# Performance work log

Measured on AMD Instinct MI355X. Metric: run time of the kernel, lower is better.

The kernel has to match this reference:

```python
import jax, jax.numpy as jnp
import numpy as np

OCC_SIZE = (200, 200, 16)  # n_query = 640000
N_CAM, C, H, W = 6, 128, 64, 176


def setup_inputs() -> dict:
    key = jax.random.key(0)
    k1, k2, k3 = jax.random.split(key, 3)
    n_query = OCC_SIZE[0] * OCC_SIZE[1] * OCC_SIZE[2]
    img_feats = jax.random.normal(k1, (N_CAM, C, H, W), dtype=jnp.float32)
    # pixel coords: x in [0, W-1], y in [0, H-1] (in-range, as the torch code assumes)
    uv = jax.random.uniform(k2, (N_CAM, n_query, 2), dtype=jnp.float32)
    points = uv * jnp.array([W - 1, H - 1], dtype=jnp.float32)
    valid = jax.random.bernoulli(k3, 0.3, (N_CAM, n_query))
    return {"img_feats": img_feats, "points": points, "valid": valid}


def reference(img_feats, points, valid):
    # Faithful to fast_voxel_fill: sequential per-camera masked writes mean the
    n_cam, n_channels = img_feats.shape[0], img_feats.shape[1]
    n_query = points.shape[-2]
    x = jnp.round(points[..., 0]).astype(jnp.int32)  # [n_cam, n_query] -> W index
    y = jnp.round(points[..., 1]).astype(jnp.int32)  # [n_cam, n_query] -> H index
    cam_ids = jnp.arange(n_cam, dtype=jnp.int32)[:, None]
    sel = jnp.max(jnp.where(valid, cam_ids, -1), axis=0)  # [n_query], -1 = no valid cam
    any_valid = sel >= 0
    cam = jnp.maximum(sel, 0)
    q = jnp.arange(n_query)
    xs = x[cam, q]
    ys = y[cam, q]
    gathered = img_feats[cam, :, ys, xs]  # [n_query, C]
    volume = jnp.where(any_valid[:, None], gathered, 0.0).T  # [C, n_query]
    return volume.reshape(n_channels, OCC_SIZE[0], OCC_SIZE[1], OCC_SIZE[2])
```

## Files before the change

kernel.cpp:

```cpp
#include <hip/hip_runtime.h>

#define NCAM 6
#define CCH  128
#define IH   64
#define IW   176
#define NQ   640000
#define PIX  (IH * IW)
#define QT   32
#define LSTRIDE 129

typedef float f32x2 __attribute__((ext_vector_type(2)));
typedef float f32x4 __attribute__((ext_vector_type(4)));

__global__ __launch_bounds__(256) void transpose_kernel(
    const float* __restrict__ in, float* __restrict__ out) {
    __shared__ float tile[32][33];
    const int cam   = blockIdx.z;
    const int pbase = blockIdx.x * 32;
    const int cbase = blockIdx.y * 32;
    const int tx = threadIdx.x, ty = threadIdx.y;

    const float* src = in  + (size_t)cam * CCH * PIX;
    float*       dst = out + (size_t)cam * PIX * CCH;

    #pragma unroll
    for (int j = 0; j < 4; ++j) {
        int c = cbase + ty + j * 8;
        tile[ty + j * 8][tx] =
            __builtin_nontemporal_load(&src[(size_t)c * PIX + (pbase + tx)]);
    }
    __syncthreads();
    #pragma unroll
    for (int j = 0; j < 4; ++j) {
        int p = pbase + ty + j * 8;
        dst[(size_t)p * CCH + (cbase + tx)] = tile[tx][ty + j * 8];
    }
}

__global__ __launch_bounds__(256, 8) void gather_lds_kernel(
    const float* __restrict__ imgT,
    const float* __restrict__ points,
    const int*   __restrict__ valid,
    float*       __restrict__ out) {
    __shared__ float feat[QT * LSTRIDE];
    __shared__ int   sbase[QT];
    __shared__ float sscale[QT];

    const int t     = threadIdx.x;
    const int qbase = blockIdx.x * QT;

    if (t < QT) {
        const int q = qbase + t;
        int sel = -1;
        #pragma unroll
        for (int cam = 0; cam < NCAM; ++cam)
            if (__builtin_nontemporal_load(&valid[(size_t)cam * NQ + q]) != 0)
                sel = cam;
        const int cam = (sel >= 0) ? sel : 0;
        sscale[t] = (sel >= 0) ? 1.0f : 0.0f;
        const f32x2 pt = __builtin_nontemporal_load(
            (const f32x2*)points + (size_t)cam * NQ + q);
        const int x = __float2int_rn(pt.x);
        const int y = __float2int_rn(pt.y);
        sbase[t] = ((cam * IH + y) * IW + x) * CCH;
    }
    __syncthreads();

    {
        const int grp  = t >> 5;
        const int lane = t & 31;
        #pragma unroll
        for (int i = 0; i < 4; ++i) {
            const int ql = i * 8 + grp;
            const float s = sscale[ql];
            const f32x4 v = *((const f32x4*)(imgT + sbase[ql]) + lane);
            const int w = ql * LSTRIDE + 4 * lane;
            feat[w + 0] = v.x * s;
            feat[w + 1] = v.y * s;
            feat[w + 2] = v.z * s;
            feat[w + 3] = v.w * s;
        }
    }
    __syncthreads();

    {
        const int l    = t & 63;
        const int wv   = t >> 6;
        const int qq   = l & 7;
        const int csub = l >> 3;
        #pragma unroll
        for (int iter = 0; iter < 4; ++iter) {
            const int c    = iter * 32 + wv * 8 + csub;
            const int qoff = 4 * qq;
            f32x4 v;
            v.x = feat[(qoff + 0) * LSTRIDE + c];
            v.y = feat[(qoff + 1) * LSTRIDE + c];
            v.z = feat[(qoff + 2) * LSTRIDE + c];
            v.w = feat[(qoff + 3) * LSTRIDE + c];
            __builtin_nontemporal_store(
                v, (f32x4*)(out + (size_t)c * NQ + qbase + qoff));
        }
    }
}

__global__ __launch_bounds__(256) void gather_direct_kernel(
    const float* __restrict__ img,
    const float* __restrict__ points,
    const int*   __restrict__ valid,
    float*       __restrict__ out) {
    const int q = blockIdx.x * 256 + threadIdx.x;

    int sel = -1;
    #pragma unroll
    for (int cam = 0; cam < NCAM; ++cam)
        if (valid[(size_t)cam * NQ + q] != 0) sel = cam;

    const float scale = (sel >= 0) ? 1.0f : 0.0f;
    const int cam = (sel >= 0) ? sel : 0;

    const float2 pt = ((const float2*)points)[(size_t)cam * NQ + q];
    const int x = __float2int_rn(pt.x);
    const int y = __float2int_rn(pt.y);

    const float* src = img + ((size_t)cam * CCH * IH + y) * IW + x;
    #pragma unroll 8
    for (int c = 0; c < CCH; ++c)
        out[(size_t)c * NQ + q] = src[(size_t)c * PIX] * scale;
}

extern "C" void kernel_launch(void* const* d_in, const int* in_sizes, int n_in,
                              void* d_out, int out_size, void* d_ws, size_t ws_size,
                              hipStream_t stream) {
    const float* img    = (const float*)d_in[0];
    const float* points = (const float*)d_in[1];
    const int*   valid  = (const int*)  d_in[2];
    float*       out    = (float*)d_out;

    const size_t need = (size_t)NCAM * CCH * IH * IW * sizeof(float);
    if (ws_size >= need) {
        float* imgT = (float*)d_ws;
        dim3 tb(32, 8, 1);
        dim3 tg(PIX / 32, CCH / 32, NCAM);
        transpose_kernel<<<tg, tb, 0, stream>>>(img, imgT);
        gather_lds_kernel<<<NQ / QT, 256, 0, stream>>>(imgT, points, valid, out);
    } else {
        gather_direct_kernel<<<NQ / 256, 256, 0, stream>>>(img, points, valid, out);
    }
}
```

Baseline: 416.2 us.

## Double-buffer gather tiles so gather loads overlap transposed output stores

Turns the one-tile-per-block gather into a persistent loop in which each block handles 8 query tiles. Two LDS buffers let the next tile's index resolution and global gathers be issued before the current tile's transposed output is stored. The aim is to hide gather latency behind store traffic and cut block launch overhead. The cost is a doubled LDS footprint, occupancy lowered to 4 blocks, and a grid eight times smaller. Any race on the shared buffers is avoided only by the single barrier in each iteration.

New measurement: 436.6 us. 4.9% more time.

```diff
diff --git a/kernel.cpp b/kernel.cpp
--- a/kernel.cpp
+++ b/kernel.cpp
@@ -7,6 +7,8 @@
 #define NQ   640000
 #define PIX  (IH * IW)
 #define QT   32
+#define NT   8
+#define NBLK (NQ / (QT * NT))
 #define LSTRIDE 129
 
 typedef float f32x2 __attribute__((ext_vector_type(2)));
@@ -37,69 +39,92 @@
     }
 }
 
-__global__ __launch_bounds__(256, 8) void gather_lds_kernel(
+__global__ __launch_bounds__(256, 4) void gather_pipe_kernel(
     const float* __restrict__ imgT,
     const float* __restrict__ points,
     const int*   __restrict__ valid,
     float*       __restrict__ out) {
-    __shared__ float feat[QT * LSTRIDE];
-    __shared__ int   sbase[QT];
-    __shared__ float sscale[QT];
+    __shared__ float feat[2][QT * LSTRIDE];
+    __shared__ int   sbase[2][QT];
+    __shared__ float sscale[2][QT];
 
     const int t     = threadIdx.x;
-    const int qbase = blockIdx.x * QT;
+    const int grp   = t >> 5;
+    const int lane  = t & 31;
+    const int tile0 = blockIdx.x * NT;
 
-    if (t < QT) {
-        const int q = qbase + t;
+    auto resolve = [&](int tile, int slot) {
+        const int q = tile * QT + t;
         int sel = -1;
         #pragma unroll
         for (int cam = 0; cam < NCAM; ++cam)
             if (__builtin_nontemporal_load(&valid[(size_t)cam * NQ + q]) != 0)
                 sel = cam;
         const int cam = (sel >= 0) ? sel : 0;
-        sscale[t] = (sel >= 0) ? 1.0f : 0.0f;
+        sscale[slot][t] = (sel >= 0) ? 1.0f : 0.0f;
         const f32x2 pt = __builtin_nontemporal_load(
             (const f32x2*)points + (size_t)cam * NQ + q);
         const int x = __float2int_rn(pt.x);
         const int y = __float2int_rn(pt.y);
-        sbase[t] = ((cam * IH + y) * IW + x) * CCH;
-    }
-    __syncthreads();
+        sbase[slot][t] = ((cam * IH + y) * IW + x) * CCH;
+    };
 
-    {
-        const int grp  = t >> 5;
-        const int lane = t & 31;
+    f32x4 r[4];
+
+    auto issue = [&](int slot) {
         #pragma unroll
         for (int i = 0; i < 4; ++i) {
             const int ql = i * 8 + grp;
-            const float s = sscale[ql];
-            const f32x4 v = *((const f32x4*)(imgT + sbase[ql]) + lane);
+            r[i] = *((const f32x4*)(imgT + sbase[slot][ql]) + lane);
+        }
+    };
+    auto commit = [&](int slot) {
+        #pragma unroll
+        for (int i = 0; i < 4; ++i) {
+            const int ql = i * 8 + grp;
+            const float s = sscale[slot][ql];
             const int w = ql * LSTRIDE + 4 * lane;
-            feat[w + 0] = v.x * s;
-            feat[w + 1] = v.y * s;
-            feat[w + 2] = v.z * s;
-            feat[w + 3] = v.w * s;
+            feat[slot][w + 0] = r[i].x * s;
+            feat[slot][w + 1] = r[i].y * s;
+            feat[slot][w + 2] = r[i].z * s;
+            feat[slot][w + 3] = r[i].w * s;
         }
-    }
+    };
+
+    if (t < QT) resolve(tile0, 0);
     __syncthreads();
+    issue(0);
+    commit(0);
 
-    {
-        const int l    = t & 63;
-        const int wv   = t >> 6;
-        const int qq   = l & 7;
-        const int csub = l >> 3;
-        #pragma unroll
-        for (int iter = 0; iter < 4; ++iter) {
-            const int c    = iter * 32 + wv * 8 + csub;
-            const int qoff = 4 * qq;
-            f32x4 v;
-            v.x = feat[(qoff + 0) * LSTRIDE + c];
-            v.y = feat[(qoff + 1) * LSTRIDE + c];
-            v.z = feat[(qoff + 2) * LSTRIDE + c];
-            v.w = feat[(qoff + 3) * LSTRIDE + c];
-            __builtin_nontemporal_store(
-                v, (f32x4*)(out + (size_t)c * NQ + qbase + qoff));
+    int cur = 0;
+    for (int tt = 0; tt < NT; ++tt) {
+        const int nxt = cur ^ 1;
+        if (tt + 1 < NT && t < QT) resolve(tile0 + tt + 1, nxt);
+        __syncthreads();
+        if (tt + 1 < NT) issue(nxt);
+
+        {
+            const int qbase = (tile0 + tt) * QT;
+            const int l    = t & 63;
+            const int wv   = t >> 6;
+            const int qq   = l & 7;
+            const int csub = l >> 3;
+            #pragma unroll
+            for (int iter = 0; iter < 4; ++iter) {
+                const int c    = iter * 32 + wv * 8 + csub;
+                const int qoff = 4 * qq;
+                f32x4 v;
+                v.x = feat[cur][(qoff + 0) * LSTRIDE + c];
+                v.y = feat[cur][(qoff + 1) * LSTRIDE + c];
+                v.z = feat[cur][(qoff + 2) * LSTRIDE + c];
+                v.w = feat[cur][(qoff + 3) * LSTRIDE + c];
+                __builtin_nontemporal_store(
+                    v, (f32x4*)(out + (size_t)c * NQ + qbase + qoff));
+            }
         }
+
+        if (tt + 1 < NT) commit(nxt);
+        cur = nxt;
     }
 }
 
@@ -142,7 +167,7 @@
         dim3 tb(32, 8, 1);
         dim3 tg(PIX / 32, CCH / 32, NCAM);
         transpose_kernel<<<tg, tb, 0, stream>>>(img, imgT);
-        gather_lds_kernel<<<NQ / QT, 256, 0, stream>>>(imgT, points, valid, out);
+        gather_pipe_kernel<<<NBLK, 256, 0, stream>>>(imgT, points, valid, out);
     } else {
         gather_direct_kernel<<<NQ / 256, 256, 0, stream>>>(img, points, valid, out);
     }
```

## Widen gather tile to 128 queries and stage channels in two halves

Applied to the files above, without the earlier changes.

The gather kernel now handles 128 queries per 512-thread block instead of 32 per 256. It stages the 128 channels in two 64-channel halves through a smaller padded LDS tile. Each output row write becomes a 256-byte contiguous segment per channel instead of 128 bytes, which should improve store coalescing for the output-bound transpose-scatter. The cost is an extra pair of barriers per half, plus the per-query setup still being done by only 128 threads.

Measured after the change: 407.9 us. 2.0% less time.

```diff
diff --git a/kernel.cpp b/kernel.cpp
--- a/kernel.cpp
+++ b/kernel.cpp
@@ -6,8 +6,9 @@
 #define IW   176
 #define NQ   640000
 #define PIX  (IH * IW)
-#define QT   32
-#define LSTRIDE 129
+#define QT   128
+#define CHALF 64
+#define FSTR  67
 
 typedef float f32x2 __attribute__((ext_vector_type(2)));
 typedef float f32x4 __attribute__((ext_vector_type(4)));
@@ -37,12 +38,12 @@
     }
 }
 
-__global__ __launch_bounds__(256, 8) void gather_lds_kernel(
+__global__ __launch_bounds__(512, 8) void gather_wide_kernel(
     const float* __restrict__ imgT,
     const float* __restrict__ points,
     const int*   __restrict__ valid,
     float*       __restrict__ out) {
-    __shared__ float feat[QT * LSTRIDE];
+    __shared__ float feat[QT * FSTR];
     __shared__ int   sbase[QT];
     __shared__ float sscale[QT];
 
@@ -66,40 +67,46 @@
     }
     __syncthreads();
 
-    {
-        const int grp  = t >> 5;
-        const int lane = t & 31;
+    const int grp16  = t >> 4;
+    const int lane16 = t & 15;
+    const int l      = t & 63;
+    const int wv     = t >> 6;
+    const int qq     = l & 15;
+    const int csub   = l >> 4;
+
+    #pragma unroll
+    for (int h = 0; h < 2; ++h) {
         #pragma unroll
         for (int i = 0; i < 4; ++i) {
-            const int ql = i * 8 + grp;
+            const int ql = i * 32 + grp16;
             const float s = sscale[ql];
-            const f32x4 v = *((const f32x4*)(imgT + sbase[ql]) + lane);
-            const int w = ql * LSTRIDE + 4 * lane;
+            const f32x4 v =
+                *((const f32x4*)(imgT + sbase[ql] + h * CHALF) + lane16);
+            const int w = ql * FSTR + 4 * lane16;
             feat[w + 0] = v.x * s;
             feat[w + 1] = v.y * s;
             feat[w + 2] = v.z * s;
             feat[w + 3] = v.w * s;
         }
-    }
-    __syncthreads();
+        __syncthreads();
 
-    {
-        const int l    = t & 63;
-        const int wv   = t >> 6;
-        const int qq   = l & 7;
-        const int csub = l >> 3;
         #pragma unroll
-        for (int iter = 0; iter < 4; ++iter) {
-            const int c    = iter * 32 + wv * 8 + csub;
-            const int qoff = 4 * qq;
-            f32x4 v;
-            v.x = feat[(qoff + 0) * LSTRIDE + c];
-            v.y = feat[(qoff + 1) * LSTRIDE + c];
-            v.z = feat[(qoff + 2) * LSTRIDE + c];
-            v.w = feat[(qoff + 3) * LSTRIDE + c];
-            __builtin_nontemporal_store(
-                v, (f32x4*)(out + (size_t)c * NQ + qbase + qoff));
+        for (int qh = 0; qh < 2; ++qh) {
+            #pragma unroll
+            for (int iter = 0; iter < 2; ++iter) {
+                const int cl   = iter * 32 + wv * 4 + csub;
+                const int c    = h * CHALF + cl;
+                const int qoff = qh * 64 + 4 * qq;
+                f32x4 v;
+                v.x = feat[(qoff + 0) * FSTR + cl];
+                v.y = feat[(qoff + 1) * FSTR + cl];
+                v.z = feat[(qoff + 2) * FSTR + cl];
+                v.w = feat[(qoff + 3) * FSTR + cl];
+                __builtin_nontemporal_store(
+                    v, (f32x4*)(out + (size_t)c * NQ + qbase + qoff));
+            }
         }
+        __syncthreads();
     }
 }
 
@@ -142,7 +149,7 @@
         dim3 tb(32, 8, 1);
         dim3 tg(PIX / 32, CCH / 32, NCAM);
         transpose_kernel<<<tg, tb, 0, stream>>>(img, imgT);
-        gather_lds_kernel<<<NQ / QT, 256, 0, stream>>>(imgT, points, valid, out);
+        gather_wide_kernel<<<NQ / QT, 512, 0, stream>>>(imgT, points, valid, out);
     } else {
         gather_direct_kernel<<<NQ / 256, 256, 0, stream>>>(img, points, valid, out);
     }
```
